# Optimization experiments

Measured on AMD Instinct MI355X. Metric: run time of the kernel, lower is better.

The kernel has to match this reference:

```python
import jax, jax.numpy as jnp
import numpy as np

B, S, IN, H, Q, M, K = 32, 2048, 128, 256, 16, 64, 3


def setup_inputs() -> dict:
    key = jax.random.key(0)
    ks = jax.random.split(key, 12)
    rn = lambda k, shp, s=0.05: (jax.random.normal(k, shp, jnp.float32) * s)
    return {
        "input_sequence": rn(ks[0], (B, S, IN), 1.0),
        "W_ih0": rn(ks[1], (4 * H, IN)),
        "W_hh0": rn(ks[2], (4 * H, H)),
        "b_ih0": jnp.zeros((4 * H,), jnp.float32),
        "b_hh0": jnp.zeros((4 * H,), jnp.float32),
        "W_ih1": rn(ks[3], (4 * H, H)),
        "W_hh1": rn(ks[4], (4 * H, H)),
        "b_ih1": jnp.zeros((4 * H,), jnp.float32),
        "b_hh1": jnp.zeros((4 * H,), jnp.float32),
        "W_cq": rn(ks[5], (Q, H)),
        "b_cq": jnp.zeros((Q,), jnp.float32),
        "mem_keys": rn(ks[6], (M, Q), 1.0),
        "mem_vals": rn(ks[7], (M, H), 1.0),
        "W_out": rn(ks[8], (H, 2 * H)),
        "b_out": jnp.zeros((H,), jnp.float32),
        "classical_weight": jnp.float32(0.7),
        "quantum_weight": jnp.float32(0.3),
    }


def _lstm_layer(x, W_ih, W_hh, b_ih, b_hh):
    """PyTorch-convention LSTM layer (gate order i,f,g,o), batch_first input."""
    Bb = x.shape[0]
    Hh = W_hh.shape[1]
    # precompute the input contribution for all timesteps: [B,S,4H]
    xg = jnp.einsum('bsi,gi->bsg', x, W_ih) + b_ih + b_hh

    def step(carry, xt):
        h, c = carry
        g = xt + h @ W_hh.T  # [B,4H]
        i, f, gg, o = jnp.split(g, 4, axis=-1)
        i = jax.nn.sigmoid(i)
        f = jax.nn.sigmoid(f)
        gg = jnp.tanh(gg)
        o = jax.nn.sigmoid(o)
        c = f * c + i * gg
        h = o * jnp.tanh(c)
        return (h, c), h

    init = (jnp.zeros((Bb, Hh), x.dtype), jnp.zeros((Bb, Hh), x.dtype))
    _, hs = jax.lax.scan(step, init, jnp.swapaxes(xg, 0, 1))  # [S,B,H]
    return jnp.swapaxes(hs, 0, 1)


def _forward(input_sequence, W_ih0, W_hh0, b_ih0, b_hh0, W_ih1, W_hh1, b_ih1,
             b_hh1, W_cq, b_cq, mem_keys, mem_vals, W_out, b_out,
             classical_weight, quantum_weight):
    # classical 2-layer LSTM
    h1 = _lstm_layer(input_sequence, W_ih0, W_hh0, b_ih0, b_hh0)
    lstm_out = _lstm_layer(h1, W_ih1, W_hh1, b_ih1, b_hh1)  # [B,S,H]

    # classical_to_quantum + tanh -> per-token query [B,S,Q]
    q = jnp.tanh(jnp.einsum('bsh,qh->bsq', lstm_out, W_cq) + b_cq)

    # batched k-NN read over the quantum memory (cosine similarity, k=3)
    eps = jnp.float32(1e-8)
    qn = q / (jnp.linalg.norm(q, axis=-1, keepdims=True) + eps)
    kn = mem_keys / (jnp.linalg.norm(mem_keys, axis=-1, keepdims=True) + eps)
    sims = jnp.einsum('bsq,mq->bsm', qn, kn)          # [B,S,M]
    top_vals, top_idx = jax.lax.top_k(sims, K)        # [B,S,K]
    gathered = mem_vals[top_idx]                      # [B,S,K,H]

    # similarity-weighted average of retrieved contents
    tot = jnp.sum(top_vals, axis=-1, keepdims=True)   # [B,S,1]
    weighted = jnp.einsum('bsk,bskh->bsh', top_vals, gathered)
    enhanced = jnp.where(tot > 0, weighted / jnp.where(tot == 0, 1.0, tot), 0.0)

    # combine streams and project
    combined = jnp.concatenate(
        [classical_weight * lstm_out, quantum_weight * enhanced], axis=-1)
    out = jnp.einsum('bsc,hc->bsh', combined, W_out) + b_out  # [B,S,H]
    return out


def reference(input_sequence, W_ih0, W_hh0, b_ih0, b_hh0, W_ih1, W_hh1, b_ih1,
              b_hh1, W_cq, b_cq, mem_keys, mem_vals, W_out, b_out,
              classical_weight, quantum_weight):
    return _forward(input_sequence, W_ih0, W_hh0, b_ih0, b_hh0, W_ih1, W_hh1,
                    b_ih1, b_hh1, W_cq, b_cq, mem_keys, mem_vals, W_out, b_out,
                    classical_weight, quantum_weight)
```

## Files before the change

### kernel.cpp

```cpp
#include <hip/hip_runtime.h>
#include <cstdint>
#include <cstddef>
#include <math.h>

#define B_   32
#define S_   2048
#define IN_  128
#define H_   256
#define Q_   16
#define M_   64
#define D_   4

__device__ __forceinline__ float4 ld4(const float* p) { return *(const float4*)p; }

#define AGLD(p)    __hip_atomic_load((p),  __ATOMIC_RELAXED, __HIP_MEMORY_SCOPE_AGENT)
#define AGST(p, v) __hip_atomic_store((p), (v), __ATOMIC_RELAXED, __HIP_MEMORY_SCOPE_AGENT)

__global__ __launch_bounds__(256, 1) void lstm2(
    const float* __restrict__ x,
    const float* __restrict__ Wih0, const float* __restrict__ bih0,
    const float* __restrict__ bhh0, const float* __restrict__ Whh0,
    const float* __restrict__ Wih1, const float* __restrict__ bih1,
    const float* __restrict__ bhh1, const float* __restrict__ Whh1,
    float* __restrict__ out,
    unsigned int* __restrict__ ex)
{
  const int f = blockIdx.x;
  const int n = (f >> 3) & 7;
  const int b = (f >> 6) * 8 + (f & 7);

  const int tid = threadIdx.x;
  const int w   = tid >> 6;
  const int l   = tid & 63;
  const int kc  = l & 7;
  const int rg  = l >> 3;
  const int wrg = w * 8 + rg;
  const int col = n * 32 + wrg;

  __shared__ float w1[128][257];
  __shared__ float aring[8][256];
  __shared__ float hring[2][256];
  __shared__ float x_sh[2][IN_];

#pragma unroll
  for (int s2 = 0; s2 < 8; s2++) aring[s2][tid] = 0.0f;
  hring[0][tid] = 0.0f;
  hring[1][tid] = 0.0f;

  float4 wf0[4][8], wf1[4][8], wi0[4][4];
  float rb0[4], rb1[4];
#pragma unroll
  for (int g = 0; g < 4; g++) {
    const int row = g * 256 + col;
    const float* p0 = Whh0 + (size_t)row * 256 + 4 * kc;
    const float* p1 = Whh1 + (size_t)row * 256 + 4 * kc;
    const float* pi = Wih0 + (size_t)row * 128 + 4 * kc;
#pragma unroll
    for (int j = 0; j < 8; j++) {
      wf0[g][j] = ld4(p0 + 32 * j);
      wf1[g][j] = ld4(p1 + 32 * j);
    }
#pragma unroll
    for (int j = 0; j < 4; j++) wi0[g][j] = ld4(pi + 32 * j);
    rb0[g] = bih0[row] + bhh0[row];
    rb1[g] = bih1[row] + bhh1[row];
    const float* pw = Wih1 + (size_t)row * 256 + 4 * kc;
    float* dst = &w1[g * 32 + wrg][4 * kc];
#pragma unroll
    for (int j = 0; j < 8; j++) *(float4*)(dst + 32 * j) = ld4(pw + 32 * j);
  }

  const float* xrow = x + (size_t)b * S_ * IN_;
  float* outp = out + (size_t)b * S_ * H_;
  unsigned int* exb = ex + (size_t)b * 2048;

  if (tid < IN_) {
    x_sh[0][tid] = xrow[tid];
    x_sh[1][tid] = xrow[IN_ + tid];
  }
  float xreg = (tid < IN_) ? xrow[(size_t)2 * IN_ + tid] : 0.0f;
  float cst0 = 0.0f, cst1 = 0.0f;
  float xa0s[4], xa1s[4] = {0, 0, 0, 0};
  __syncthreads();

  {
    const float* xb = x_sh[0];
    float4 xv[4];
#pragma unroll
    for (int j = 0; j < 4; j++) xv[j] = ld4(xb + 4 * kc + 32 * j);
#pragma unroll
    for (int g = 0; g < 4; g++) {
      float4 s4 = {0, 0, 0, 0};
#pragma unroll
      for (int j = 0; j < 4; j++) {
        s4.x += wi0[g][j].x * xv[j].x; s4.y += wi0[g][j].y * xv[j].y;
        s4.z += wi0[g][j].z * xv[j].z; s4.w += wi0[g][j].w * xv[j].w;
      }
      float s = (s4.x + s4.y) + (s4.z + s4.w);
      s += __shfl_xor(s, 1); s += __shfl_xor(s, 2); s += __shfl_xor(s, 4);
      xa0s[g] = s + rb0[g];
    }
  }

  bool dead = false;
  for (int t = 0; t < S_ + D_; ++t) {
    const bool doA = (t < S_);
    const int  u   = t - D_;
    const bool doH = (u >= 0);

    if (doA) {
      const float* ap = aring[(t - 1) & 7];
      float4 av[8];
#pragma unroll
      for (int j = 0; j < 8; j++) av[j] = ld4(ap + 4 * kc + 32 * j);
      float gv[4];
#pragma unroll
      for (int g = 0; g < 4; g++) {
        float4 s4 = {0, 0, 0, 0};
#pragma unroll
        for (int j = 0; j < 8; j++) {
          s4.x += wf0[g][j].x * av[j].x; s4.y += wf0[g][j].y * av[j].y;
          s4.z += wf0[g][j].z * av[j].z; s4.w += wf0[g][j].w * av[j].w;
        }
        float s = (s4.x + s4.y) + (s4.z + s4.w);
        s += __shfl_xor(s, 1); s += __shfl_xor(s, 2); s += __shfl_xor(s, 4);
        gv[g] = s + xa0s[g];
      }
      float ig = 1.0f / (1.0f + expf(-gv[0]));
      float fg = 1.0f / (1.0f + expf(-gv[1]));
      float cg = tanhf(gv[2]);
      float og = 1.0f / (1.0f + expf(-gv[3]));
      cst0 = fg * cst0 + ig * cg;
      float a = og * tanhf(cst0);
      if (kc == 0) {
        unsigned bits = __float_as_uint(a);
        unsigned tag  = (unsigned)(t + 1) << 16;
        const int p = t & 1;
        AGST(exb + (((0 * 2 + p) * 2 + 0) << 8) + col, tag | (bits >> 16));
        AGST(exb + (((0 * 2 + p) * 2 + 1) << 8) + col, tag | (bits & 0xffffu));
      }
    }
    if (doH) {
      const float* hp = hring[(t - 1) & 1];
      float4 hv[8];
#pragma unroll
      for (int j = 0; j < 8; j++) hv[j] = ld4(hp + 4 * kc + 32 * j);
      float gv[4];
#pragma unroll
      for (int g = 0; g < 4; g++) {
        float4 s4 = {0, 0, 0, 0};
#pragma unroll
        for (int j = 0; j < 8; j++) {
          s4.x += wf1[g][j].x * hv[j].x; s4.y += wf1[g][j].y * hv[j].y;
          s4.z += wf1[g][j].z * hv[j].z; s4.w += wf1[g][j].w * hv[j].w;
        }
        float s = (s4.x + s4.y) + (s4.z + s4.w);
        s += __shfl_xor(s, 1); s += __shfl_xor(s, 2); s += __shfl_xor(s, 4);
        gv[g] = s + xa1s[g];
      }
      float ig = 1.0f / (1.0f + expf(-gv[0]));
      float fg = 1.0f / (1.0f + expf(-gv[1]));
      float cg = tanhf(gv[2]);
      float og = 1.0f / (1.0f + expf(-gv[3]));
      cst1 = fg * cst1 + ig * cg;
      float h = og * tanhf(cst1);
      if (kc == 0) {
        outp[(size_t)u * H_ + col] = h;
        unsigned bits = __float_as_uint(h);
        unsigned tag  = (unsigned)(u + 1) << 16;
        const int p = u & 1;
        AGST(exb + (((1 * 2 + p) * 2 + 0) << 8) + col, tag | (bits >> 16));
        AGST(exb + (((1 * 2 + p) * 2 + 1) << 8) + col, tag | (bits & 0xffffu));
      }
    }

    if (t + 1 < S_) {
      const float* xb = x_sh[(t + 1) & 1];
      float4 xv[4];
#pragma unroll
      for (int j = 0; j < 4; j++) xv[j] = ld4(xb + 4 * kc + 32 * j);
#pragma unroll
      for (int g = 0; g < 4; g++) {
        float4 s4 = {0, 0, 0, 0};
#pragma unroll
        for (int j = 0; j < 4; j++) {
          s4.x += wi0[g][j].x * xv[j].x; s4.y += wi0[g][j].y * xv[j].y;
          s4.z += wi0[g][j].z * xv[j].z; s4.w += wi0[g][j].w * xv[j].w;
        }
        float s = (s4.x + s4.y) + (s4.z + s4.w);
        s += __shfl_xor(s, 1); s += __shfl_xor(s, 2); s += __shfl_xor(s, 4);
        xa0s[g] = s + rb0[g];
      }
    }
    {
      const int v = t - D_ + 1;
      if (v >= 0 && v < S_) {
        const float* avp = aring[v & 7];
        float4 av[8];
#pragma unroll
        for (int j = 0; j < 8; j++) av[j] = ld4(avp + 4 * kc + 32 * j);
#pragma unroll
        for (int g = 0; g < 4; g++) {
          const float* wr = &w1[g * 32 + wrg][4 * kc];
          float4 s4 = {0, 0, 0, 0};
#pragma unroll
          for (int j = 0; j < 8; j++) {
            float4 wv = ld4(wr + 32 * j);
            s4.x += wv.x * av[j].x; s4.y += wv.y * av[j].y;
            s4.z += wv.z * av[j].z; s4.w += wv.w * av[j].w;
          }
          float s = (s4.x + s4.y) + (s4.z + s4.w);
          s += __shfl_xor(s, 1); s += __shfl_xor(s, 2); s += __shfl_xor(s, 4);
          xa1s[g] = s + rb1[g];
        }
      }
    }
    float xreg_n = 0.0f;
    if (tid < IN_ && t + 2 < S_) {
      int tn = (t + 3 < S_) ? t + 3 : S_ - 1;
      xreg_n = xrow[(size_t)tn * IN_ + tid];
    }

    if (!dead && (doA || doH)) {
      const unsigned eA = (unsigned)(t + 1) & 0xffffu;
      const unsigned eH = (unsigned)(u + 1) & 0xffffu;
      const int pa = t & 1, ph = u & 1;
      unsigned int* aHi = exb + (((0 * 2 + pa) * 2 + 0) << 8) + tid;
      unsigned int* aLo = exb + (((0 * 2 + pa) * 2 + 1) << 8) + tid;
      unsigned int* hHi = exb + (((1 * 2 + ph) * 2 + 0) << 8) + tid;
      unsigned int* hLo = exb + (((1 * 2 + ph) * 2 + 1) << 8) + tid;
      unsigned a0v = 0, a1v = 0, h0v = 0, h1v = 0;
      bool needA = doA, needH = doH;
      unsigned guard = 0;
      while (true) {
        if (needA) {
          a0v = AGLD(aHi); a1v = AGLD(aLo);
          if ((a0v >> 16) == eA && (a1v >> 16) == eA) needA = false;
        }
        if (needH) {
          h0v = AGLD(hHi); h1v = AGLD(hLo);
          if ((h0v >> 16) == eH && (h1v >> 16) == eH) needH = false;
        }
        if (!needA && !needH) break;
        if (++guard >= (1u << 20)) { dead = true; break; }
      }
      if (doA) aring[t & 7][tid] = __uint_as_float((a0v << 16) | (a1v & 0xffffu));
      if (doH) hring[t & 1][tid] = __uint_as_float((h0v << 16) | (h1v & 0xffffu));
    }
    if (tid < IN_ && t < S_) x_sh[t & 1][tid] = xreg;
    xreg = xreg_n;
    __syncthreads();
  }
}

__global__ __launch_bounds__(256) void knn_enh(
    const float* __restrict__ lstm, const float* __restrict__ Wcq,
    const float* __restrict__ bcq, const float* __restrict__ keys,
    const float* __restrict__ vals, const float* __restrict__ qwp,
    float* __restrict__ enh)
{
  const int tid  = threadIdx.x;
  const int wave = tid >> 6, lane = tid & 63;
  const int t = blockIdx.x * 4 + wave;

  __shared__ float xsh[4][256];
  __shared__ float qsh[4][16];

  const float* xrow = lstm + (size_t)t * H_;
  float4 x4 = ld4(xrow + lane * 4);
  *(float4*)&xsh[wave][lane * 4] = x4;
  __syncthreads();

  const int j = lane & 15, seg = lane >> 4;
  const float* wrow = Wcq + j * H_ + seg * 64;
  const float* xseg = &xsh[wave][seg * 64];
  float p = 0.0f;
#pragma unroll
  for (int c = 0; c < 64; c += 4) {
    float4 w4 = ld4(wrow + c);
    p += w4.x * xseg[c] + w4.y * xseg[c + 1] + w4.z * xseg[c + 2] + w4.w * xseg[c + 3];
  }
  p += __shfl_xor(p, 16);
  p += __shfl_xor(p, 32);
  float q = tanhf(p + bcq[j]);

  float sq = q * q;
  sq += __shfl_xor(sq, 1); sq += __shfl_xor(sq, 2);
  sq += __shfl_xor(sq, 4); sq += __shfl_xor(sq, 8);
  float qn = q / (sqrtf(sq) + 1e-8f);
  if (lane < 16) qsh[wave][lane] = qn;
  __syncthreads();

  const int m = lane;
  const float* krow = keys + m * Q_;
  float kv[16]; float kn2 = 0.0f;
#pragma unroll
  for (int jj = 0; jj < 16; jj++) { kv[jj] = krow[jj]; kn2 += kv[jj] * kv[jj]; }
  float rn = 1.0f / (sqrtf(kn2) + 1e-8f);
  float sim = 0.0f;
#pragma unroll
  for (int jj = 0; jj < 16; jj++) sim += qsh[wave][jj] * kv[jj];
  sim *= rn;

  float rem = sim;
  float tv[3]; int ti[3];
#pragma unroll
  for (int k = 0; k < 3; k++) {
    float v = rem; int idx = m;
#pragma unroll
    for (int d = 1; d < 64; d <<= 1) {
      float ov = __shfl_xor(v, d);
      int   oi = __shfl_xor(idx, d);
      if (ov > v || (ov == v && oi < idx)) { v = ov; idx = oi; }
    }
    tv[k] = v; ti[k] = idx;
    if (m == idx) rem = -INFINITY;
  }
  float tot = tv[0] + tv[1] + tv[2];

  float ex = 0, ey = 0, ez = 0, ew = 0;
#pragma unroll
  for (int k = 0; k < 3; k++) {
    float4 vv = ld4(vals + (size_t)ti[k] * H_ + lane * 4);
    ex += tv[k] * vv.x; ey += tv[k] * vv.y;
    ez += tv[k] * vv.z; ew += tv[k] * vv.w;
  }
  float inv = (tot > 0.0f) ? 1.0f / tot : 0.0f;
  const float qw = qwp[0];

  float4 o;
  o.x = qw * ex * inv; o.y = qw * ey * inv;
  o.z = qw * ez * inv; o.w = qw * ew * inv;
  *(float4*)&enh[(size_t)t * H_ + lane * 4] = o;
}

__global__ __launch_bounds__(256) void gemm_cat(
    float* __restrict__ io, const float* __restrict__ A2,
    const float* __restrict__ Bw, const float* __restrict__ bias,
    const float* __restrict__ cwp)
{
  __shared__ float As[16][68];
  __shared__ float Bs[16][260];
  const int tid  = threadIdx.x;
  const int row0 = blockIdx.x * 64;
  const int tx = tid & 15, ty = tid >> 4;
  const int lr = tid >> 2;
  const int lk = (tid & 3) << 2;
  const float cw = cwp[0];

  float acc[4][16];
#pragma unroll
  for (int i = 0; i < 4; i++)
#pragma unroll
    for (int j = 0; j < 16; j++) acc[i][j] = 0.0f;

  for (int k0 = 0; k0 < 512; k0 += 16) {
    float4 av;
    if (k0 < 256) {
      av = ld4(io + (size_t)(row0 + lr) * 256 + k0 + lk);
      av.x *= cw; av.y *= cw; av.z *= cw; av.w *= cw;
    } else {
      av = ld4(A2 + (size_t)(row0 + lr) * 256 + (k0 - 256) + lk);
    }
    As[lk + 0][lr] = av.x; As[lk + 1][lr] = av.y;
    As[lk + 2][lr] = av.z; As[lk + 3][lr] = av.w;
    const float* bp = Bw + (size_t)tid * 512 + k0;
#pragma unroll
    for (int q = 0; q < 4; q++) {
      float4 b4 = ld4(bp + 4 * q);
      Bs[4 * q + 0][tid] = b4.x; Bs[4 * q + 1][tid] = b4.y;
      Bs[4 * q + 2][tid] = b4.z; Bs[4 * q + 3][tid] = b4.w;
    }
    __syncthreads();
#pragma unroll
    for (int k = 0; k < 16; k++) {
      float4 a4 = *(const float4*)&As[k][ty << 2];
      float aa[4] = {a4.x, a4.y, a4.z, a4.w};
#pragma unroll
      for (int cc = 0; cc < 4; cc++) {
        float4 b4 = *(const float4*)&Bs[k][cc * 64 + (tx << 2)];
        float bb[4] = {b4.x, b4.y, b4.z, b4.w};
#pragma unroll
        for (int i = 0; i < 4; i++)
#pragma unroll
          for (int jj = 0; jj < 4; jj++) acc[i][cc * 4 + jj] += aa[i] * bb[jj];
      }
    }
    __syncthreads();
  }

#pragma unroll
  for (int i = 0; i < 4; i++) {
#pragma unroll
    for (int cc = 0; cc < 4; cc++) {
      int c0 = cc * 64 + (tx << 2);
      float4 o;
      o.x = acc[i][cc * 4 + 0] + bias[c0 + 0];
      o.y = acc[i][cc * 4 + 1] + bias[c0 + 1];
      o.z = acc[i][cc * 4 + 2] + bias[c0 + 2];
      o.w = acc[i][cc * 4 + 3] + bias[c0 + 3];
      *(float4*)&io[(size_t)(row0 + (ty << 2) + i) * 256 + c0] = o;
    }
  }
}

extern "C" void kernel_launch(void* const* d_in, const int* in_sizes, int n_in,
                              void* d_out, int out_size, void* d_ws, size_t ws_size,
                              hipStream_t stream)
{
  const float* x    = (const float*)d_in[0];
  const float* Wih0 = (const float*)d_in[1];
  const float* Whh0 = (const float*)d_in[2];
  const float* bih0 = (const float*)d_in[3];
  const float* bhh0 = (const float*)d_in[4];
  const float* Wih1 = (const float*)d_in[5];
  const float* Whh1 = (const float*)d_in[6];
  const float* bih1 = (const float*)d_in[7];
  const float* bhh1 = (const float*)d_in[8];
  const float* Wcq  = (const float*)d_in[9];
  const float* bcq  = (const float*)d_in[10];
  const float* keys = (const float*)d_in[11];
  const float* vals = (const float*)d_in[12];
  const float* Wout = (const float*)d_in[13];
  const float* bout = (const float*)d_in[14];
  const float* cw   = (const float*)d_in[15];
  const float* qw   = (const float*)d_in[16];
  float* out = (float*)d_out;

  const size_t HE = (size_t)B_ * S_ * H_;
  if (ws_size < HE * sizeof(float)) return;
  unsigned int* ex = (unsigned int*)d_ws;
  float* enh = (float*)d_ws;

  const int MT = B_ * S_;
  dim3 blk(256);

  hipMemsetAsync(ex, 0, (size_t)32 * 2048 * sizeof(unsigned int), stream);
  lstm2<<<dim3(256), blk, 0, stream>>>(x, Wih0, bih0, bhh0, Whh0,
                                       Wih1, bih1, bhh1, Whh1, out, ex);

  knn_enh<<<dim3(MT / 4), blk, 0, stream>>>(out, Wcq, bcq, keys, vals, qw, enh);

  gemm_cat<<<dim3(MT / 64), blk, 0, stream>>>(out, enh, Wout, bout, cw);
}
```

Baseline: 14.47 ms.

## Use 64-bit tagged exchange with volatile fast path and local-slice bypass

Replaces the split 16-bit hi/lo tagged exchange with single 64-bit words that hold a 32-bit tag plus the full float, so each inter-block handoff needs one load instead of two. It adds a second, volatile-written exchange buffer that consumers poll a few times before falling back to agent-scope atomic loads. Each block writes its own slice of the recurrent state directly to shared memory and skips polling for it. The block-to-batch mapping changes so the eight column blocks of one batch are spaced 32 apart, and the activations switch to fast __expf-based sigmoid and tanh, trading a little accuracy for cheaper math. The volatile fast path relies on cache visibility across blocks, which is a coherence risk.

```diff
diff --git a/kernel.cpp b/kernel.cpp
--- a/kernel.cpp
+++ b/kernel.cpp
@@ -11,10 +11,15 @@
 #define M_   64
 #define D_   4
 
+typedef unsigned long long u64;
+
 __device__ __forceinline__ float4 ld4(const float* p) { return *(const float4*)p; }
 
-#define AGLD(p)    __hip_atomic_load((p),  __ATOMIC_RELAXED, __HIP_MEMORY_SCOPE_AGENT)
-#define AGST(p, v) __hip_atomic_store((p), (v), __ATOMIC_RELAXED, __HIP_MEMORY_SCOPE_AGENT)
+#define AGLD64(p)    __hip_atomic_load((p),  __ATOMIC_RELAXED, __HIP_MEMORY_SCOPE_AGENT)
+#define AGST64(p, v) __hip_atomic_store((p), (v), __ATOMIC_RELAXED, __HIP_MEMORY_SCOPE_AGENT)
+
+__device__ __forceinline__ float sigm_f(float x) { return 1.0f / (1.0f + __expf(-x)); }
+__device__ __forceinline__ float tanh_f(float x) { return 1.0f - 2.0f / (__expf(2.0f * x) + 1.0f); }
 
 __global__ __launch_bounds__(256, 1) void lstm2(
     const float* __restrict__ x,
@@ -23,11 +28,12 @@
     const float* __restrict__ Wih1, const float* __restrict__ bih1,
     const float* __restrict__ bhh1, const float* __restrict__ Whh1,
     float* __restrict__ out,
-    unsigned int* __restrict__ ex)
+    u64* __restrict__ exs,
+    u64* __restrict__ exf)
 {
   const int f = blockIdx.x;
-  const int n = (f >> 3) & 7;
-  const int b = (f >> 6) * 8 + (f & 7);
+  const int n = f >> 5;
+  const int b = f & 31;
 
   const int tid = threadIdx.x;
   const int w   = tid >> 6;
@@ -72,7 +78,8 @@
 
   const float* xrow = x + (size_t)b * S_ * IN_;
   float* outp = out + (size_t)b * S_ * H_;
-  unsigned int* exb = ex + (size_t)b * 2048;
+  u64* sexb = exs + (size_t)b * 1024;
+  volatile u64* fexb = (volatile u64*)(exf + (size_t)b * 1024);
 
   if (tid < IN_) {
     x_sh[0][tid] = xrow[tid];
@@ -102,11 +109,13 @@
     }
   }
 
+  const bool own = ((tid >> 5) == n);
   bool dead = false;
   for (int t = 0; t < S_ + D_; ++t) {
     const bool doA = (t < S_);
     const int  u   = t - D_;
     const bool doH = (u >= 0);
+    const int  pa = t & 1, ph = u & 1;
 
     if (doA) {
       const float* ap = aring[(t - 1) & 7];
@@ -126,18 +135,17 @@
         s += __shfl_xor(s, 1); s += __shfl_xor(s, 2); s += __shfl_xor(s, 4);
         gv[g] = s + xa0s[g];
       }
-      float ig = 1.0f / (1.0f + expf(-gv[0]));
-      float fg = 1.0f / (1.0f + expf(-gv[1]));
-      float cg = tanhf(gv[2]);
-      float og = 1.0f / (1.0f + expf(-gv[3]));
+      float ig = sigm_f(gv[0]);
+      float fg = sigm_f(gv[1]);
+      float cg = tanh_f(gv[2]);
+      float og = sigm_f(gv[3]);
       cst0 = fg * cst0 + ig * cg;
-      float a = og * tanhf(cst0);
+      float a = og * tanh_f(cst0);
       if (kc == 0) {
-        unsigned bits = __float_as_uint(a);
-        unsigned tag  = (unsigned)(t + 1) << 16;
-        const int p = t & 1;
-        AGST(exb + (((0 * 2 + p) * 2 + 0) << 8) + col, tag | (bits >> 16));
-        AGST(exb + (((0 * 2 + p) * 2 + 1) << 8) + col, tag | (bits & 0xffffu));
+        u64 pk = ((u64)(unsigned)(t + 1) << 32) | (u64)__float_as_uint(a);
+        fexb[((0 * 2 + pa) << 8) + col] = pk;
+        AGST64(sexb + ((0 * 2 + pa) << 8) + col, pk);
+        aring[t & 7][col] = a;
       }
     }
     if (doH) {
@@ -158,21 +166,29 @@
         s += __shfl_xor(s, 1); s += __shfl_xor(s, 2); s += __shfl_xor(s, 4);
         gv[g] = s + xa1s[g];
       }
-      float ig = 1.0f / (1.0f + expf(-gv[0]));
-      float fg = 1.0f / (1.0f + expf(-gv[1]));
-      float cg = tanhf(gv[2]);
-      float og = 1.0f / (1.0f + expf(-gv[3]));
+      float ig = sigm_f(gv[0]);
+      float fg = sigm_f(gv[1]);
+      float cg = tanh_f(gv[2]);
+      float og = sigm_f(gv[3]);
       cst1 = fg * cst1 + ig * cg;
-      float h = og * tanhf(cst1);
+      float h = og * tanh_f(cst1);
       if (kc == 0) {
         outp[(size_t)u * H_ + col] = h;
-        unsigned bits = __float_as_uint(h);
-        unsigned tag  = (unsigned)(u + 1) << 16;
-        const int p = u & 1;
-        AGST(exb + (((1 * 2 + p) * 2 + 0) << 8) + col, tag | (bits >> 16));
-        AGST(exb + (((1 * 2 + p) * 2 + 1) << 8) + col, tag | (bits & 0xffffu));
-      }
-    }
+        u64 pk = ((u64)(unsigned)(u + 1) << 32) | (u64)__float_as_uint(h);
+        fexb[((1 * 2 + ph) << 8) + col] = pk;
+        AGST64(sexb + ((1 * 2 + ph) << 8) + col, pk);
+        hring[u & 1][col] = h;
+      }
+    }
+
+    bool needA = doA && !own && !dead;
+    bool needH = doH && !own && !dead;
+    const unsigned eA = (unsigned)(t + 1), eH = (unsigned)(u + 1);
+    volatile u64* fA = fexb + ((0 * 2 + pa) << 8) + tid;
+    volatile u64* fH = fexb + ((1 * 2 + ph) << 8) + tid;
+    u64 vA = 0, vH = 0;
+    if (needA) vA = *fA;
+    if (needH) vH = *fH;
 
     if (t + 1 < S_) {
       const float* xb = x_sh[(t + 1) & 1];
@@ -221,32 +237,26 @@
       xreg_n = xrow[(size_t)tn * IN_ + tid];
     }
 
-    if (!dead && (doA || doH)) {
-      const unsigned eA = (unsigned)(t + 1) & 0xffffu;
-      const unsigned eH = (unsigned)(u + 1) & 0xffffu;
-      const int pa = t & 1, ph = u & 1;
-      unsigned int* aHi = exb + (((0 * 2 + pa) * 2 + 0) << 8) + tid;
-      unsigned int* aLo = exb + (((0 * 2 + pa) * 2 + 1) << 8) + tid;
-      unsigned int* hHi = exb + (((1 * 2 + ph) * 2 + 0) << 8) + tid;
-      unsigned int* hLo = exb + (((1 * 2 + ph) * 2 + 1) << 8) + tid;
-      unsigned a0v = 0, a1v = 0, h0v = 0, h1v = 0;
-      bool needA = doA, needH = doH;
+    if (needA && (unsigned)(vA >> 32) == eA) needA = false;
+    if (needH && (unsigned)(vH >> 32) == eH) needH = false;
+#pragma unroll 1
+    for (int spin = 0; (needA || needH) && spin < 6; ++spin) {
+      if (needA) { vA = *fA; if ((unsigned)(vA >> 32) == eA) needA = false; }
+      if (needH) { vH = *fH; if ((unsigned)(vH >> 32) == eH) needH = false; }
+    }
+    if (needA || needH) {
+      u64* sA = sexb + ((0 * 2 + pa) << 8) + tid;
+      u64* sH = sexb + ((1 * 2 + ph) << 8) + tid;
       unsigned guard = 0;
-      while (true) {
-        if (needA) {
-          a0v = AGLD(aHi); a1v = AGLD(aLo);
-          if ((a0v >> 16) == eA && (a1v >> 16) == eA) needA = false;
-        }
-        if (needH) {
-          h0v = AGLD(hHi); h1v = AGLD(hLo);
-          if ((h0v >> 16) == eH && (h1v >> 16) == eH) needH = false;
-        }
-        if (!needA && !needH) break;
+      while (needA || needH) {
+        if (needA) { vA = AGLD64(sA); if ((unsigned)(vA >> 32) == eA) needA = false; }
+        if (needH) { vH = AGLD64(sH); if ((unsigned)(vH >> 32) == eH) needH = false; }
         if (++guard >= (1u << 20)) { dead = true; break; }
       }
-      if (doA) aring[t & 7][tid] = __uint_as_float((a0v << 16) | (a1v & 0xffffu));
-      if (doH) hring[t & 1][tid] = __uint_as_float((h0v << 16) | (h1v & 0xffffu));
-    }
+    }
+    if (doA && !own) aring[t & 7][tid] = __uint_as_float((unsigned)vA);
+    if (doH && !own) hring[u & 1][tid] = __uint_as_float((unsigned)vH);
+
     if (tid < IN_ && t < S_) x_sh[t & 1][tid] = xreg;
     xreg = xreg_n;
     __syncthreads();
@@ -429,15 +439,16 @@
 
   const size_t HE = (size_t)B_ * S_ * H_;
   if (ws_size < HE * sizeof(float)) return;
-  unsigned int* ex = (unsigned int*)d_ws;
+  u64* exs = (u64*)d_ws;
+  u64* exf = exs + (size_t)32 * 1024;
   float* enh = (float*)d_ws;
 
   const int MT = B_ * S_;
   dim3 blk(256);
 
-  hipMemsetAsync(ex, 0, (size_t)32 * 2048 * sizeof(unsigned int), stream);
+  hipMemsetAsync(exs, 0, (size_t)2 * 32 * 1024 * sizeof(u64), stream);
   lstm2<<<dim3(256), blk, 0, stream>>>(x, Wih0, bih0, bhh0, Whh0,
-                                       Wih1, bih1, bhh1, Whh1, out, ex);
+                                       Wih1, bih1, bhh1, Whh1, out, exs, exf);
 
   knn_enh<<<dim3(MT / 4), blk, 0, stream>>>(out, Wcq, bcq, keys, vals, qw, enh);
 
```

Measured after the change: 15.89 ms. 1.1x slower.
